# Kernel tuning notes

Hardware: AMD Instinct MI355X
Metric: run time of the kernel (lower is better)

Reference implementation:

```python
import jax, jax.numpy as jnp
import numpy as np
import math

N_HEAD = 16

def _rope_tables(seq, dh, dtype):
    inv_freq = 1.0 / (10000.0 ** (jnp.arange(0, dh, 2, dtype=jnp.float32) / dh))
    angle = jnp.arange(seq, dtype=jnp.float32)[:, None] * inv_freq[None, :]  # [S, dh/2]
    sin = jnp.repeat(jnp.sin(angle), 2, axis=-1).astype(dtype)  # [S, dh]
    cos = jnp.repeat(jnp.cos(angle), 2, axis=-1).astype(dtype)
    return sin, cos

def _rotate_half(x):
    x_even = x[..., ::2]
    x_odd = x[..., 1::2]
    return jnp.stack([-x_odd, x_even], axis=-1).reshape(x.shape)

def _apply_rope(x, sin, cos):
    # x: [B, H, S, dh]; sin/cos: [S, dh]
    return x * cos[None, None] + _rotate_half(x) * sin[None, None]

def setup_inputs() -> dict:
    key = jax.random.key(0)
    ks = jax.random.split(key, 9)
    B, S, D = 2, 2048, 2048
    scale = 1.0 / math.sqrt(D)
    x = jax.random.normal(ks[0], (B, S, D), dtype=jnp.float32)
    wq = jax.random.normal(ks[1], (D, D), dtype=jnp.float32) * scale
    wk = jax.random.normal(ks[2], (D, D), dtype=jnp.float32) * scale
    wv = jax.random.normal(ks[3], (D, D), dtype=jnp.float32) * scale
    wo = jax.random.normal(ks[4], (D, D), dtype=jnp.float32) * scale
    bq = jnp.zeros((D,), jnp.float32)
    bk = jnp.zeros((D,), jnp.float32)
    bv = jnp.zeros((D,), jnp.float32)
    bo = jnp.zeros((D,), jnp.float32)
    # causal mask: True = masked (strict upper triangle)
    mask = jnp.triu(jnp.ones((S, S), dtype=bool), k=1)[None, None]  # [1,1,S,S]
    return {"x": x, "wq": wq, "bq": bq, "wk": wk, "bk": bk, "wv": wv, "bv": bv,
            "wo": wo, "bo": bo, "mask": mask}

def reference(x, wq, bq, wk, bk, wv, bv, wo, bo, mask):
    B, S, D = x.shape
    H = N_HEAD
    dh = D // H
    # projections (torch Linear: x @ W.T + b)
    q = (x @ wq.T + bq).reshape(B, S, H, dh).transpose(0, 2, 1, 3)  # [B,H,S,dh]
    k = (x @ wk.T + bk).reshape(B, S, H, dh).transpose(0, 2, 1, 3)
    v = (x @ wv.T + bv).reshape(B, S, H, dh).transpose(0, 2, 1, 3)
    sin, cos = _rope_tables(S, dh, x.dtype)
    q = _apply_rope(q, sin, cos)
    k = _apply_rope(k, sin, cos)
    scores = jnp.einsum('bhqd,bhkd->bhqk', q, k) / math.sqrt(dh)
    scores = jnp.where(mask, -jnp.inf, scores)
    attn = jax.nn.softmax(scores, axis=-1)
    attn = jnp.nan_to_num(attn, nan=0.0)
    out = jnp.einsum('bhqk,bhkd->bhqd', attn, v)  # [B,H,S,dh]
    out = out.transpose(0, 2, 1, 3).reshape(B, S, D)
    return out @ wo.T + bo
```

## Files before the change

kernel.cpp:

```cpp
#include <hip/hip_runtime.h>
#include <math.h>


typedef _Float16 half8 __attribute__((ext_vector_type(8)));
typedef _Float16 half4v __attribute__((ext_vector_type(4)));
typedef float f32x4 __attribute__((ext_vector_type(4)));

__device__ __forceinline__ void gl_lds16(const void* g, void* l) {
  __builtin_amdgcn_global_load_lds(
      (const __attribute__((address_space(1))) unsigned int*)g,
      (__attribute__((address_space(3))) unsigned int*)l, 16, 0, 0);
}

__global__ void cast_f32_f16(const float* __restrict__ src, _Float16* __restrict__ dst, int n4) {
  int i = blockIdx.x * blockDim.x + threadIdx.x;
  if (i >= n4) return;
  float4 v = reinterpret_cast<const float4*>(src)[i];
  half4v o;
  o[0] = (_Float16)v.x; o[1] = (_Float16)v.y; o[2] = (_Float16)v.z; o[3] = (_Float16)v.w;
  reinterpret_cast<half4v*>(dst)[i] = o;
}

__global__ void cast_w(const float* __restrict__ w0, const float* __restrict__ w1,
                       const float* __restrict__ w2, const float* __restrict__ w3,
                       _Float16* __restrict__ wdst) {
  const float* s = blockIdx.y == 0 ? w0 : blockIdx.y == 1 ? w1 : blockIdx.y == 2 ? w2 : w3;
  int i = blockIdx.x * blockDim.x + threadIdx.x;
  float4 v = reinterpret_cast<const float4*>(s)[i];
  half4v o;
  o[0] = (_Float16)v.x; o[1] = (_Float16)v.y; o[2] = (_Float16)v.z; o[3] = (_Float16)v.w;
  reinterpret_cast<half4v*>(wdst)[(size_t)blockIdx.y * 1048576 + i] = o;
}

template <bool OUT_F32>
__global__ __launch_bounds__(512, 2) void gemm_bt256(
    const _Float16* __restrict__ A,
    const _Float16* __restrict__ B,
    const float* __restrict__ b0, const float* __restrict__ b1,
    const float* __restrict__ b2,
    void* __restrict__ Cout,
    int M, int N, int K) {
  __shared__ _Float16 As[2][16384];
  __shared__ _Float16 Bs[2][16384];
  const int bm = blockIdx.y * 256, bn = blockIdx.x * 256;
  const int tid = threadIdx.x;
  const int wave = tid >> 6, lane = tid & 63;
  const int quad = lane >> 4, l16 = lane & 15;
  const int wm = (wave >> 2) * 128, wn = (wave & 3) * 64;

  const int srow = tid >> 3;
  const int sx = (tid & 7) ^ (srow & 7);
  const _Float16* Ag = A + (size_t)(bm + srow) * K + sx * 8;
  const _Float16* Bg[4];
#pragma unroll
  for (int c = 0; c < 4; ++c) {
    int r = (((c * 2 + (srow >> 5)) & 3) << 6) + ((c >> 1) << 5) + (srow & 31);
    Bg[c] = B + (size_t)(bn + r) * K + sx * 8;
  }

#define STAGE_A(buf, R, kt) \
  gl_lds16(Ag + (size_t)(R) * K + (kt) * 64, &As[buf][(R) * 64 + tid * 8])
#define STAGE_B(buf, c, kt) \
  gl_lds16(Bg[c] + (kt) * 64, &Bs[buf][(c) * 4096 + tid * 8])

  const int axor = l16 & 7;
  const int sl0 = ((0 + quad) ^ axor) * 8;
  const int sl1 = ((4 + quad) ^ axor) * 8;
  const int aoff = (wm + l16) * 64;
  const int q4 = (wn >> 6) * 32;

#define RD_A(i, kk) \
  (*reinterpret_cast<const half8*>(&As[cur][aoff + (i) * 1024 + ((kk) ? sl1 : sl0)]))
#define RD_B(j, kk) \
  (*reinterpret_cast<const half8*>( \
      &Bs[cur][((((j) >> 1) * 128 + q4 + ((j) & 1) * 16 + l16)) * 64 + ((kk) ? sl1 : sl0)]))

  f32x4 acc[8][4];
#pragma unroll
  for (int i = 0; i < 8; ++i)
#pragma unroll
    for (int j = 0; j < 4; ++j) acc[i][j] = f32x4{0.f, 0.f, 0.f, 0.f};

  half8 a[4][2], b[4][2];
  const int NT = K >> 6;

  STAGE_A(0, 0, 0); STAGE_A(0, 128, 0);
  STAGE_B(0, 0, 0); STAGE_B(0, 1, 0);
  STAGE_B(0, 2, 0); STAGE_B(0, 3, 0);
  STAGE_A(0, 64, 0); STAGE_A(0, 192, 0);
  if (NT > 1) {
    STAGE_A(1, 0, 1); STAGE_A(1, 128, 1);
    STAGE_B(1, 0, 1); STAGE_B(1, 1, 1);
    STAGE_B(1, 2, 1); STAGE_B(1, 3, 1);
    asm volatile("s_waitcnt vmcnt(6)");
  } else {
    asm volatile("s_waitcnt vmcnt(0)");
  }
  __builtin_amdgcn_s_barrier();

  for (int t = 0; t < NT; ++t) {
    const int cur = t & 1, nxt = cur ^ 1;
    const bool pf1 = (t + 1 < NT);
    const bool pf2 = (t + 2 < NT);

#pragma unroll
    for (int i = 0; i < 4; ++i) {
      a[i][0] = RD_A(i, 0); a[i][1] = RD_A(i, 1);
    }
#pragma unroll
    for (int j = 0; j < 2; ++j) {
      b[j][0] = RD_B(j, 0); b[j][1] = RD_B(j, 1);
    }
    if (pf1) { STAGE_A(nxt, 64, t + 1); STAGE_A(nxt, 192, t + 1); }
    __builtin_amdgcn_s_barrier();
    __builtin_amdgcn_s_setprio(1);
#pragma unroll
    for (int i = 0; i < 4; ++i)
#pragma unroll
      for (int j = 0; j < 2; ++j) {
        acc[i][j] = __builtin_amdgcn_mfma_f32_16x16x32_f16(a[i][0], b[j][0], acc[i][j], 0, 0, 0);
        acc[i][j] = __builtin_amdgcn_mfma_f32_16x16x32_f16(a[i][1], b[j][1], acc[i][j], 0, 0, 0);
      }
    __builtin_amdgcn_s_setprio(0);
    __builtin_amdgcn_s_barrier();

#pragma unroll
    for (int j = 2; j < 4; ++j) {
      b[j][0] = RD_B(j, 0); b[j][1] = RD_B(j, 1);
    }
    if (pf2) { STAGE_A(cur, 0, t + 2); STAGE_A(cur, 128, t + 2); }
    __builtin_amdgcn_s_barrier();
    __builtin_amdgcn_s_setprio(1);
#pragma unroll
    for (int i = 0; i < 4; ++i)
#pragma unroll
      for (int j = 2; j < 4; ++j) {
        acc[i][j] = __builtin_amdgcn_mfma_f32_16x16x32_f16(a[i][0], b[j][0], acc[i][j], 0, 0, 0);
        acc[i][j] = __builtin_amdgcn_mfma_f32_16x16x32_f16(a[i][1], b[j][1], acc[i][j], 0, 0, 0);
      }
    __builtin_amdgcn_s_setprio(0);
    __builtin_amdgcn_s_barrier();

#pragma unroll
    for (int i = 0; i < 4; ++i) {
      a[i][0] = RD_A(i + 4, 0); a[i][1] = RD_A(i + 4, 1);
    }
    if (pf2) { STAGE_B(cur, 0, t + 2); STAGE_B(cur, 1, t + 2); }
    __builtin_amdgcn_s_barrier();
    __builtin_amdgcn_s_setprio(1);
#pragma unroll
    for (int i = 0; i < 4; ++i)
#pragma unroll
      for (int j = 0; j < 2; ++j) {
        acc[i + 4][j] = __builtin_amdgcn_mfma_f32_16x16x32_f16(a[i][0], b[j][0], acc[i + 4][j], 0, 0, 0);
        acc[i + 4][j] = __builtin_amdgcn_mfma_f32_16x16x32_f16(a[i][1], b[j][1], acc[i + 4][j], 0, 0, 0);
      }
    __builtin_amdgcn_s_setprio(0);
    __builtin_amdgcn_s_barrier();

    if (pf2) { STAGE_B(cur, 2, t + 2); STAGE_B(cur, 3, t + 2); }
    __builtin_amdgcn_s_barrier();
    __builtin_amdgcn_s_setprio(1);
#pragma unroll
    for (int i = 0; i < 4; ++i)
#pragma unroll
      for (int j = 2; j < 4; ++j) {
        acc[i + 4][j] = __builtin_amdgcn_mfma_f32_16x16x32_f16(a[i][0], b[j][0], acc[i + 4][j], 0, 0, 0);
        acc[i + 4][j] = __builtin_amdgcn_mfma_f32_16x16x32_f16(a[i][1], b[j][1], acc[i + 4][j], 0, 0, 0);
      }
    __builtin_amdgcn_s_setprio(0);
    if (pf2)
      asm volatile("s_waitcnt vmcnt(6)");
    else
      asm volatile("s_waitcnt vmcnt(0)");
    __builtin_amdgcn_s_barrier();
  }

#pragma unroll
  for (int j = 0; j < 4; ++j) {
    const int gc = bn + wn + j * 16 + l16;
    const float* bp = (gc < 2048) ? b0 : (gc < 4096 ? b1 : b2);
    const float bz = bp[gc & 2047];
#pragma unroll
    for (int i = 0; i < 8; ++i) {
#pragma unroll
      for (int r = 0; r < 4; ++r) {
        const int gr = bm + wm + i * 16 + quad * 4 + r;
        float v = acc[i][j][r] + bz;
        if (OUT_F32)
          reinterpret_cast<float*>(Cout)[(size_t)gr * N + gc] = v;
        else
          reinterpret_cast<_Float16*>(Cout)[(size_t)gr * N + gc] = (_Float16)v;
      }
    }
  }
#undef STAGE_A
#undef STAGE_B
#undef RD_A
#undef RD_B
}

__global__ void rope_inplace(_Float16* __restrict__ qkv, int ngroups) {
  int idx = blockIdx.x * blockDim.x + threadIdx.x;
  if (idx >= ngroups) return;
  int m = idx >> 8;
  int g = idx & 255;
  int s = m & 2047;
  const float scale = 0.088388347648318447f;
  size_t base = (size_t)m * 6144 + g * 8;
  half8 qv = *reinterpret_cast<const half8*>(qkv + base);
  half8 kv = *reinterpret_cast<const half8*>(qkv + base + 2048);
  half8 qo, ko;
#pragma unroll
  for (int j = 0; j < 4; ++j) {
    int i = (g * 4 + j) & 63;
    float ang = (float)s * exp2f(-0.2076205059304601f * (float)i);
    float sn, cs;
    __sincosf(ang, &sn, &cs);
    float e = (float)qv[j * 2], o = (float)qv[j * 2 + 1];
    qo[j * 2]     = (_Float16)((e * cs - o * sn) * scale);
    qo[j * 2 + 1] = (_Float16)((o * cs + e * sn) * scale);
    e = (float)kv[j * 2]; o = (float)kv[j * 2 + 1];
    ko[j * 2]     = (_Float16)(e * cs - o * sn);
    ko[j * 2 + 1] = (_Float16)(o * cs + e * sn);
  }
  *reinterpret_cast<half8*>(qkv + base) = qo;
  *reinterpret_cast<half8*>(qkv + base + 2048) = ko;
}

__global__ __launch_bounds__(256) void transpose_v(const _Float16* __restrict__ qkv,
                                                   _Float16* __restrict__ vt) {
  __shared__ _Float16 t[64][72];
  const int s0 = blockIdx.x * 64;
  const int d0 = blockIdx.y * 64;
  const int bh = blockIdx.z;
  const int b = bh >> 4, h = bh & 15;
  const int tid = threadIdx.x;
#pragma unroll
  for (int p = 0; p < 2; ++p) {
    int chunk = p * 256 + tid;
    int r = chunk >> 3, c8 = (chunk & 7) * 8;
    *reinterpret_cast<half8*>(&t[r][c8]) = *reinterpret_cast<const half8*>(
        &qkv[(size_t)(b * 2048 + s0 + r) * 6144 + 4096 + h * 128 + d0 + c8]);
  }
  __syncthreads();
#pragma unroll
  for (int p = 0; p < 2; ++p) {
    int chunk = p * 256 + tid;
    int dr = chunk >> 3, c8 = (chunk & 7) * 8;
    half8 o;
#pragma unroll
    for (int j = 0; j < 8; ++j) o[j] = t[c8 + j][dr];
    *reinterpret_cast<half8*>(&vt[(size_t)(bh * 128 + d0 + dr) * 2048 + s0 + c8]) = o;
  }
}

__global__ __launch_bounds__(256, 2) void attn_kernel(
    const _Float16* __restrict__ QKV,
    const _Float16* __restrict__ VT,
    _Float16* __restrict__ ctx) {
  constexpr int LD = 6144, S = 2048;
  __shared__ _Float16 Ks[2][8192];
  __shared__ _Float16 Vs[2][8192];
  __shared__ _Float16 P[4][16][80];
  const int bid = blockIdx.x;
  const int bh = bid & 31;
  const int qt = 31 - (bid >> 5);
  const int b = bh >> 4, h = bh & 15;
  const int tid = threadIdx.x;
  const int wv = tid >> 6, lane = tid & 63;
  const int quad = lane >> 4, l16 = lane & 15;
  const int q0 = qt * 64 + wv * 16;

  const _Float16* qp = QKV + (size_t)(b * S + q0 + l16) * LD + h * 128;
  half8 aq[4];
#pragma unroll
  for (int ks = 0; ks < 4; ++ks)
    aq[ks] = *reinterpret_cast<const half8*>(qp + ks * 32 + quad * 8);

  const _Float16* gk[4];
  const _Float16* gv[4];
  int lofs[4];
#pragma unroll
  for (int p = 0; p < 4; ++p) {
    int c = p * 256 + tid;
    int cl16 = c & 15, cqd = (c >> 4) & 3;
    int cks = (c >> 6) & 3, cf = c >> 8;
    gk[p] = QKV + (size_t)(b * S + cf * 16 + cl16) * LD + 2048 + h * 128 + cks * 32 + cqd * 8;
    int ckv = (c >> 6) & 1, ct = c >> 7;
    gv[p] = VT + (size_t)(bh * 128 + ct * 16 + cl16) * S + ckv * 32 + cqd * 8;
    lofs[p] = c * 8;
  }

  f32x4 acc[8];
#pragma unroll
  for (int t = 0; t < 8; ++t) acc[t] = f32x4{0.f, 0.f, 0.f, 0.f};
  f32x4 lacc = f32x4{0.f, 0.f, 0.f, 0.f};
  float m_i[4];
#pragma unroll
  for (int r = 0; r < 4; ++r) m_i[r] = -INFINITY;

  half8 ones;
#pragma unroll
  for (int j = 0; j < 8; ++j) ones[j] = (_Float16)1.0f;

#pragma unroll
  for (int p = 0; p < 4; ++p) gl_lds16(gk[p], &Ks[0][lofs[p]]);
#pragma unroll
  for (int p = 0; p < 4; ++p) gl_lds16(gv[p], &Vs[0][lofs[p]]);

  for (int j = 0; j <= qt; ++j) {
    __syncthreads();
    const int cur = j & 1;
    if (j < qt) {
      const size_t ko = (size_t)(j + 1) * 64 * LD;
      const int vo = (j + 1) * 64;
#pragma unroll
      for (int p = 0; p < 4; ++p) gl_lds16(gk[p] + ko, &Ks[cur ^ 1][lofs[p]]);
#pragma unroll
      for (int p = 0; p < 4; ++p) gl_lds16(gv[p] + vo, &Vs[cur ^ 1][lofs[p]]);
    }
    f32x4 sf[4];
#pragma unroll
    for (int f = 0; f < 4; ++f) sf[f] = f32x4{0.f, 0.f, 0.f, 0.f};
#pragma unroll
    for (int f = 0; f < 4; ++f)
#pragma unroll
      for (int ks = 0; ks < 4; ++ks) {
        half8 bk = *reinterpret_cast<const half8*>(&Ks[cur][((f * 4 + ks) * 4 + quad) * 128 + l16 * 8]);
        sf[f] = __builtin_amdgcn_mfma_f32_16x16x32_f16(aq[ks], bk, sf[f], 0, 0, 0);
      }
    if (j == qt) {
      const int key0 = j * 64;
#pragma unroll
      for (int f = 0; f < 4; ++f) {
        const int key = key0 + f * 16 + l16;
#pragma unroll
        for (int r = 0; r < 4; ++r) {
          const int row = q0 + quad * 4 + r;
          sf[f][r] = (key <= row) ? sf[f][r] : -1e30f;
        }
      }
    }
    float alpha[4];
#pragma unroll
    for (int r = 0; r < 4; ++r) {
      float tm = fmaxf(fmaxf(sf[0][r], sf[1][r]), fmaxf(sf[2][r], sf[3][r]));
      tm = fmaxf(tm, __shfl_xor(tm, 1));
      tm = fmaxf(tm, __shfl_xor(tm, 2));
      tm = fmaxf(tm, __shfl_xor(tm, 4));
      tm = fmaxf(tm, __shfl_xor(tm, 8));
      const float mn = fmaxf(m_i[r], tm);
      alpha[r] = __expf(m_i[r] - mn);
      m_i[r] = mn;
    }
#pragma unroll
    for (int f = 0; f < 4; ++f)
#pragma unroll
      for (int r = 0; r < 4; ++r)
        P[wv][quad * 4 + r][f * 16 + l16] = (_Float16)__expf(sf[f][r] - m_i[r]);
    half8 pa0 = *reinterpret_cast<const half8*>(&P[wv][l16][quad * 8]);
    half8 pa1 = *reinterpret_cast<const half8*>(&P[wv][l16][32 + quad * 8]);
#pragma unroll
    for (int t = 0; t < 8; ++t)
#pragma unroll
      for (int r = 0; r < 4; ++r) acc[t][r] *= alpha[r];
#pragma unroll
    for (int r = 0; r < 4; ++r) lacc[r] *= alpha[r];
#pragma unroll
    for (int t = 0; t < 8; ++t) {
      half8 bv0 = *reinterpret_cast<const half8*>(&Vs[cur][((t * 2 + 0) * 4 + quad) * 128 + l16 * 8]);
      half8 bv1 = *reinterpret_cast<const half8*>(&Vs[cur][((t * 2 + 1) * 4 + quad) * 128 + l16 * 8]);
      acc[t] = __builtin_amdgcn_mfma_f32_16x16x32_f16(pa0, bv0, acc[t], 0, 0, 0);
      acc[t] = __builtin_amdgcn_mfma_f32_16x16x32_f16(pa1, bv1, acc[t], 0, 0, 0);
    }
    lacc = __builtin_amdgcn_mfma_f32_16x16x32_f16(pa0, ones, lacc, 0, 0, 0);
    lacc = __builtin_amdgcn_mfma_f32_16x16x32_f16(pa1, ones, lacc, 0, 0, 0);
  }

  float inv[4];
#pragma unroll
  for (int r = 0; r < 4; ++r) inv[r] = 1.0f / lacc[r];
#pragma unroll
  for (int t = 0; t < 8; ++t)
#pragma unroll
    for (int r = 0; r < 4; ++r)
      ctx[(size_t)(b * S + q0 + quad * 4 + r) * 2048 + h * 128 + t * 16 + l16] =
          (_Float16)(acc[t][r] * inv[r]);
}

extern "C" void kernel_launch(void* const* d_in, const int* in_sizes, int n_in,
                              void* d_out, int out_size, void* d_ws, size_t ws_size,
                              hipStream_t stream) {
  const float* x  = (const float*)d_in[0];
  const float* wq = (const float*)d_in[1];
  const float* bq = (const float*)d_in[2];
  const float* wk = (const float*)d_in[3];
  const float* bk = (const float*)d_in[4];
  const float* wv = (const float*)d_in[5];
  const float* bv = (const float*)d_in[6];
  const float* wo = (const float*)d_in[7];
  const float* bo = (const float*)d_in[8];

  _Float16* W      = (_Float16*)d_ws;
  _Float16* xh     = W;
  _Float16* wqkvh  = xh + 8388608;
  _Float16* woh    = wqkvh + 12582912;
  _Float16* qkvlin = woh + 4194304;
  _Float16* vT     = xh;
  _Float16* ctx    = wqkvh;

  cast_f32_f16<<<8192, 256, 0, stream>>>(x, xh, 2097152);
  cast_w<<<dim3(4096, 4), 256, 0, stream>>>(wq, wk, wv, wo, wqkvh);

  gemm_bt256<false><<<dim3(24, 16), 512, 0, stream>>>(xh, wqkvh, bq, bk, bv, qkvlin,
                                                      4096, 6144, 2048);

  rope_inplace<<<4096, 256, 0, stream>>>(qkvlin, 1048576);
  transpose_v<<<dim3(32, 2, 32), 256, 0, stream>>>(qkvlin, vT);
  attn_kernel<<<1024, 256, 0, stream>>>(qkvlin, vT, ctx);

  gemm_bt256<true><<<dim3(8, 16), 512, 0, stream>>>(ctx, woh, bo, bo, bo, (float*)d_out,
                                                    4096, 2048, 2048);
}
```

Measured before the change: 451.6 us.

## Switch GEMM to 32x32x16 MFMA with reworked LDS staging and XCD-aware tile remap

Rewrites the 256x256 GEMM inner loop to use 32x32x16 f16 MFMA instructions instead of 16x16x32, with a new swizzled LDS layout and fragment loads. The intent is fewer LDS reads per MFMA and higher matrix-core throughput. The pipeline is restructured so B for the next tile is prefetched first and the next iteration's A/B fragments are preloaded after the barrier, with fewer barriers per iteration. Workgroup IDs are also remapped in strides of 8 so neighbouring tiles land on the same XCD for L2 reuse. This adds risk from the more complex wait-count and barrier logic and from the new swizzle.

Measured after the change: 464.7 us. +2.9%, slower.

```diff
diff --git a/kernel.cpp b/kernel.cpp
--- a/kernel.cpp
+++ b/kernel.cpp
@@ -5,6 +5,7 @@
 typedef _Float16 half8 __attribute__((ext_vector_type(8)));
 typedef _Float16 half4v __attribute__((ext_vector_type(4)));
 typedef float f32x4 __attribute__((ext_vector_type(4)));
+typedef float f32x16 __attribute__((ext_vector_type(16)));
 
 __device__ __forceinline__ void gl_lds16(const void* g, void* l) {
   __builtin_amdgcn_global_load_lds(
@@ -36,157 +37,149 @@
 __global__ __launch_bounds__(512, 2) void gemm_bt256(
     const _Float16* __restrict__ A,
     const _Float16* __restrict__ B,
-    const float* __restrict__ b0, const float* __restrict__ b1,
-    const float* __restrict__ b2,
+    const float* __restrict__ b0p, const float* __restrict__ b1p,
+    const float* __restrict__ b2p,
     void* __restrict__ Cout,
     int M, int N, int K) {
   __shared__ _Float16 As[2][16384];
   __shared__ _Float16 Bs[2][16384];
-  const int bm = blockIdx.y * 256, bn = blockIdx.x * 256;
+  const int nwg = gridDim.x * gridDim.y;
+  int lin = blockIdx.y * gridDim.x + blockIdx.x;
+  lin = (lin & 7) * (nwg >> 3) + (lin >> 3);
+  const int bm = (lin / gridDim.x) * 256, bn = (lin % gridDim.x) * 256;
+
   const int tid = threadIdx.x;
   const int wave = tid >> 6, lane = tid & 63;
-  const int quad = lane >> 4, l16 = lane & 15;
+  const int l31 = lane & 31, hi = lane >> 5;
   const int wm = (wave >> 2) * 128, wn = (wave & 3) * 64;
 
   const int srow = tid >> 3;
   const int sx = (tid & 7) ^ (srow & 7);
   const _Float16* Ag = A + (size_t)(bm + srow) * K + sx * 8;
-  const _Float16* Bg[4];
-#pragma unroll
-  for (int c = 0; c < 4; ++c) {
-    int r = (((c * 2 + (srow >> 5)) & 3) << 6) + ((c >> 1) << 5) + (srow & 31);
-    Bg[c] = B + (size_t)(bn + r) * K + sx * 8;
-  }
-
-#define STAGE_A(buf, R, kt) \
-  gl_lds16(Ag + (size_t)(R) * K + (kt) * 64, &As[buf][(R) * 64 + tid * 8])
-#define STAGE_B(buf, c, kt) \
-  gl_lds16(Bg[c] + (kt) * 64, &Bs[buf][(c) * 4096 + tid * 8])
-
-  const int axor = l16 & 7;
-  const int sl0 = ((0 + quad) ^ axor) * 8;
-  const int sl1 = ((4 + quad) ^ axor) * 8;
-  const int aoff = (wm + l16) * 64;
-  const int q4 = (wn >> 6) * 32;
-
-#define RD_A(i, kk) \
-  (*reinterpret_cast<const half8*>(&As[cur][aoff + (i) * 1024 + ((kk) ? sl1 : sl0)]))
-#define RD_B(j, kk) \
-  (*reinterpret_cast<const half8*>( \
-      &Bs[cur][((((j) >> 1) * 128 + q4 + ((j) & 1) * 16 + l16)) * 64 + ((kk) ? sl1 : sl0)]))
-
-  f32x4 acc[8][4];
-#pragma unroll
-  for (int i = 0; i < 8; ++i)
-#pragma unroll
-    for (int j = 0; j < 4; ++j) acc[i][j] = f32x4{0.f, 0.f, 0.f, 0.f};
-
-  half8 a[4][2], b[4][2];
+  const _Float16* Bg = B + (size_t)(bn + srow) * K + sx * 8;
+
+#define STAGE_A(buf, h, kt)                                                   \
+  do {                                                                        \
+    gl_lds16(Ag + (size_t)((h) * 128) * K + (kt) * 64,                        \
+             &As[buf][(h) * 8192 + tid * 8]);                                 \
+    gl_lds16(Ag + (size_t)((h) * 128 + 64) * K + (kt) * 64,                   \
+             &As[buf][(h) * 8192 + 4096 + tid * 8]);                          \
+  } while (0)
+#define STAGE_B(buf, h, kt)                                                   \
+  do {                                                                        \
+    gl_lds16(Bg + (size_t)((h) * 128) * K + (kt) * 64,                        \
+             &Bs[buf][(h) * 8192 + tid * 8]);                                 \
+    gl_lds16(Bg + (size_t)((h) * 128 + 64) * K + (kt) * 64,                   \
+             &Bs[buf][(h) * 8192 + 4096 + tid * 8]);                          \
+  } while (0)
+
+  const int base_a = (wm + l31) * 64;
+  const int base_b = (wn + l31) * 64;
+  int sofs[4];
+#pragma unroll
+  for (int ks = 0; ks < 4; ++ks) sofs[ks] = ((ks * 2 + hi) ^ (lane & 7)) * 8;
+
+#define RD_A(buf, blk, ks) \
+  (*reinterpret_cast<const half8*>(&As[buf][base_a + (blk) * 2048 + sofs[ks]]))
+#define RD_B(buf, blk, ks) \
+  (*reinterpret_cast<const half8*>(&Bs[buf][base_b + (blk) * 2048 + sofs[ks]]))
+
+  f32x16 acc[4][2];
+#pragma unroll
+  for (int i = 0; i < 4; ++i)
+#pragma unroll
+    for (int j = 0; j < 2; ++j)
+#pragma unroll
+      for (int r = 0; r < 16; ++r) acc[i][j][r] = 0.f;
+
+  half8 a1[2][4], a2[2][4], bb0[4], bb1[4];
   const int NT = K >> 6;
 
-  STAGE_A(0, 0, 0); STAGE_A(0, 128, 0);
+  STAGE_A(0, 0, 0); STAGE_A(0, 1, 0);
   STAGE_B(0, 0, 0); STAGE_B(0, 1, 0);
-  STAGE_B(0, 2, 0); STAGE_B(0, 3, 0);
-  STAGE_A(0, 64, 0); STAGE_A(0, 192, 0);
-  if (NT > 1) {
-    STAGE_A(1, 0, 1); STAGE_A(1, 128, 1);
-    STAGE_B(1, 0, 1); STAGE_B(1, 1, 1);
-    STAGE_B(1, 2, 1); STAGE_B(1, 3, 1);
-    asm volatile("s_waitcnt vmcnt(6)");
-  } else {
-    asm volatile("s_waitcnt vmcnt(0)");
-  }
+  STAGE_A(1, 0, 1); STAGE_A(1, 1, 1);
+  asm volatile("s_waitcnt vmcnt(4)" ::: "memory");
   __builtin_amdgcn_s_barrier();
+  __builtin_amdgcn_sched_barrier(0);
+#pragma unroll
+  for (int ks = 0; ks < 4; ++ks) {
+    a1[0][ks] = RD_A(0, 0, ks);
+    bb0[ks] = RD_B(0, 0, ks);
+    a1[1][ks] = RD_A(0, 1, ks);
+  }
 
   for (int t = 0; t < NT; ++t) {
     const int cur = t & 1, nxt = cur ^ 1;
-    const bool pf1 = (t + 1 < NT);
-    const bool pf2 = (t + 2 < NT);
-
-#pragma unroll
-    for (int i = 0; i < 4; ++i) {
-      a[i][0] = RD_A(i, 0); a[i][1] = RD_A(i, 1);
-    }
-#pragma unroll
-    for (int j = 0; j < 2; ++j) {
-      b[j][0] = RD_B(j, 0); b[j][1] = RD_B(j, 1);
-    }
-    if (pf1) { STAGE_A(nxt, 64, t + 1); STAGE_A(nxt, 192, t + 1); }
-    __builtin_amdgcn_s_barrier();
+
+    if (t + 1 < NT) { STAGE_B(nxt, 0, t + 1); STAGE_B(nxt, 1, t + 1); }
+#pragma unroll
+    for (int ks = 0; ks < 4; ++ks) bb1[ks] = RD_B(cur, 1, ks);
     __builtin_amdgcn_s_setprio(1);
 #pragma unroll
-    for (int i = 0; i < 4; ++i)
-#pragma unroll
-      for (int j = 0; j < 2; ++j) {
-        acc[i][j] = __builtin_amdgcn_mfma_f32_16x16x32_f16(a[i][0], b[j][0], acc[i][j], 0, 0, 0);
-        acc[i][j] = __builtin_amdgcn_mfma_f32_16x16x32_f16(a[i][1], b[j][1], acc[i][j], 0, 0, 0);
-      }
+    for (int i = 0; i < 2; ++i)
+#pragma unroll
+      for (int ks = 0; ks < 4; ++ks)
+        acc[i][0] = __builtin_amdgcn_mfma_f32_32x32x16_f16(a1[i][ks], bb0[ks], acc[i][0], 0, 0, 0);
     __builtin_amdgcn_s_setprio(0);
     __builtin_amdgcn_s_barrier();
 
 #pragma unroll
-    for (int j = 2; j < 4; ++j) {
-      b[j][0] = RD_B(j, 0); b[j][1] = RD_B(j, 1);
-    }
-    if (pf2) { STAGE_A(cur, 0, t + 2); STAGE_A(cur, 128, t + 2); }
-    __builtin_amdgcn_s_barrier();
+    for (int i = 0; i < 2; ++i)
+#pragma unroll
+      for (int ks = 0; ks < 4; ++ks) a2[i][ks] = RD_A(cur, i + 2, ks);
     __builtin_amdgcn_s_setprio(1);
 #pragma unroll
-    for (int i = 0; i < 4; ++i)
-#pragma unroll
-      for (int j = 2; j < 4; ++j) {
-        acc[i][j] = __builtin_amdgcn_mfma_f32_16x16x32_f16(a[i][0], b[j][0], acc[i][j], 0, 0, 0);
-        acc[i][j] = __builtin_amdgcn_mfma_f32_16x16x32_f16(a[i][1], b[j][1], acc[i][j], 0, 0, 0);
-      }
+    for (int i = 0; i < 2; ++i)
+#pragma unroll
+      for (int ks = 0; ks < 4; ++ks)
+        acc[i][1] = __builtin_amdgcn_mfma_f32_32x32x16_f16(a1[i][ks], bb1[ks], acc[i][1], 0, 0, 0);
     __builtin_amdgcn_s_setprio(0);
     __builtin_amdgcn_s_barrier();
 
-#pragma unroll
-    for (int i = 0; i < 4; ++i) {
-      a[i][0] = RD_A(i + 4, 0); a[i][1] = RD_A(i + 4, 1);
-    }
-    if (pf2) { STAGE_B(cur, 0, t + 2); STAGE_B(cur, 1, t + 2); }
-    __builtin_amdgcn_s_barrier();
+    if (t + 2 < NT) { STAGE_A(cur, 0, t + 2); STAGE_A(cur, 1, t + 2); }
     __builtin_amdgcn_s_setprio(1);
 #pragma unroll
-    for (int i = 0; i < 4; ++i)
-#pragma unroll
-      for (int j = 0; j < 2; ++j) {
-        acc[i + 4][j] = __builtin_amdgcn_mfma_f32_16x16x32_f16(a[i][0], b[j][0], acc[i + 4][j], 0, 0, 0);
-        acc[i + 4][j] = __builtin_amdgcn_mfma_f32_16x16x32_f16(a[i][1], b[j][1], acc[i + 4][j], 0, 0, 0);
-      }
+    for (int i = 0; i < 2; ++i)
+#pragma unroll
+      for (int ks = 0; ks < 4; ++ks)
+        acc[i + 2][0] = __builtin_amdgcn_mfma_f32_32x32x16_f16(a2[i][ks], bb0[ks], acc[i + 2][0], 0, 0, 0);
     __builtin_amdgcn_s_setprio(0);
     __builtin_amdgcn_s_barrier();
 
-    if (pf2) { STAGE_B(cur, 2, t + 2); STAGE_B(cur, 3, t + 2); }
-    __builtin_amdgcn_s_barrier();
     __builtin_amdgcn_s_setprio(1);
 #pragma unroll
-    for (int i = 0; i < 4; ++i)
-#pragma unroll
-      for (int j = 2; j < 4; ++j) {
-        acc[i + 4][j] = __builtin_amdgcn_mfma_f32_16x16x32_f16(a[i][0], b[j][0], acc[i + 4][j], 0, 0, 0);
-        acc[i + 4][j] = __builtin_amdgcn_mfma_f32_16x16x32_f16(a[i][1], b[j][1], acc[i + 4][j], 0, 0, 0);
+    for (int i = 0; i < 2; ++i)
+#pragma unroll
+      for (int ks = 0; ks < 4; ++ks)
+        acc[i + 2][1] = __builtin_amdgcn_mfma_f32_32x32x16_f16(a2[i][ks], bb1[ks], acc[i + 2][1], 0, 0, 0);
+    __builtin_amdgcn_s_setprio(0);
+    if (t + 1 < NT) {
+      if (t + 2 < NT)
+        asm volatile("s_waitcnt vmcnt(4)" ::: "memory");
+      else
+        asm volatile("s_waitcnt vmcnt(0)" ::: "memory");
+      __builtin_amdgcn_s_barrier();
+      __builtin_amdgcn_sched_barrier(0);
+#pragma unroll
+      for (int ks = 0; ks < 4; ++ks) {
+        a1[0][ks] = RD_A(nxt, 0, ks);
+        bb0[ks] = RD_B(nxt, 0, ks);
+        a1[1][ks] = RD_A(nxt, 1, ks);
       }
-    __builtin_amdgcn_s_setprio(0);
-    if (pf2)
-      asm volatile("s_waitcnt vmcnt(6)");
-    else
-      asm volatile("s_waitcnt vmcnt(0)");
-    __builtin_amdgcn_s_barrier();
-  }
-
-#pragma unroll
-  for (int j = 0; j < 4; ++j) {
-    const int gc = bn + wn + j * 16 + l16;
-    const float* bp = (gc < 2048) ? b0 : (gc < 4096 ? b1 : b2);
+    }
+  }
+
+#pragma unroll
+  for (int j = 0; j < 2; ++j) {
+    const int gc = bn + wn + j * 32 + l31;
+    const float* bp = (gc < 2048) ? b0p : (gc < 4096 ? b1p : b2p);
     const float bz = bp[gc & 2047];
 #pragma unroll
-    for (int i = 0; i < 8; ++i) {
-#pragma unroll
-      for (int r = 0; r < 4; ++r) {
-        const int gr = bm + wm + i * 16 + quad * 4 + r;
-        float v = acc[i][j][r] + bz;
+    for (int i2 = 0; i2 < 4; ++i2) {
+#pragma unroll
+      for (int r = 0; r < 16; ++r) {
+        const int gr = bm + wm + i2 * 32 + (r & 3) + 8 * (r >> 2) + 4 * hi;
+        float v = acc[i2][j][r] + bz;
         if (OUT_F32)
           reinterpret_cast<float*>(Cout)[(size_t)gr * N + gc] = v;
         else
```
